# Kernel optimization log

Measured on AMD Instinct MI355X. Metric: run time of the kernel, lower is better.

## Reference

```python
import jax, jax.numpy as jnp
import numpy as np

DT = 1.0            # neuron_config.base_config.dt (ms)
TAU_MEM = 10.0      # membrane time constant (ms)
SURROGATE_BETA = 1.0  # surrogate sigmoid sharpness for spike nonlinearity

B, P = 256, 4096


def setup_inputs() -> dict:
    key = jax.random.key(0)
    k1, k2, k3, k4 = jax.random.split(key, 4)
    return {
        "external_input": jax.random.normal(k1, (B, P), dtype=jnp.float32),
        "lateral_weights": jax.random.normal(k2, (P, P), dtype=jnp.float32) * 0.1,
        "population_activity": jax.random.uniform(k3, (P,), dtype=jnp.float32),
        "v": jax.random.normal(k4, (B, P), dtype=jnp.float32),
        "threshold": jnp.ones((B, P), dtype=jnp.float32),
    }


def reference(external_input, lateral_weights, population_activity, v, threshold):
    P_ = external_input.shape[1]
    # lateral inhibition: zero self-connections (inhibition_mask = eye == 0)
    masked_w = lateral_weights * (1.0 - jnp.eye(P_, dtype=lateral_weights.dtype))
    lateral = population_activity @ masked_w              # [P]
    total_input = external_input - lateral[None, :]        # [B, P]
    # vectorized adaptive-threshold LIF step across the whole population
    decay = jnp.exp(jnp.asarray(-DT / TAU_MEM, dtype=v.dtype))
    v_new = decay * v + total_input                        # [B, P]
    u = (v_new - threshold) / SURROGATE_BETA
    soft = jax.nn.sigmoid(u)
    hard = (v_new > threshold).astype(v.dtype)
    # straight-through spike: hard forward, sigmoid-surrogate gradient
    spikes = jax.lax.stop_gradient(hard - soft) + soft     # [B, P]
    return spikes
```

## Files before the change

kernel.cpp:

```cpp
#include <hip/hip_runtime.h>


#define PP 4096
#define BB 256

using f4 = __attribute__((ext_vector_type(4))) float;

constexpr int ROWS_PER_CHUNK = 16;
constexpr int NCHUNK = PP / ROWS_PER_CHUNK;
constexpr int COLS_PER_TILE = 1024;
constexpr int NTILE = PP / COLS_PER_TILE;

__global__ __launch_bounds__(256)
void lateral_partial(const float* __restrict__ w, const float* __restrict__ pa,
                     double* __restrict__ part) {
    const int tile = blockIdx.x & (NTILE - 1);
    const int rch  = blockIdx.x >> 2;
    const int c    = tile * COLS_PER_TILE + (int)threadIdx.x * 4;
    const int r0   = rch * ROWS_PER_CHUNK;
    double a0 = 0.0, a1 = 0.0, a2 = 0.0, a3 = 0.0;
#pragma unroll
    for (int k = 0; k < ROWS_PER_CHUNK; ++k) {
        const int i = r0 + k;
        const double p = (double)pa[i];
        const f4 wv = __builtin_nontemporal_load(
            reinterpret_cast<const f4*>(w + (size_t)i * PP + c));
        a0 += p * (double)wv.x;
        a1 += p * (double)wv.y;
        a2 += p * (double)wv.z;
        a3 += p * (double)wv.w;
    }
    double* dst = part + (size_t)rch * PP + c;
    *reinterpret_cast<double2*>(dst)     = make_double2(a0, a1);
    *reinterpret_cast<double2*>(dst + 2) = make_double2(a2, a3);
}

__global__ __launch_bounds__(256)
void lateral_reduce(const double* __restrict__ part, const float* __restrict__ w,
                    const float* __restrict__ pa, double* __restrict__ lat) {
    __shared__ double sh[256];
    const int t   = (int)threadIdx.x;
    const int cj  = t & 7;
    const int grp = t >> 3;
    const int col = blockIdx.x * 8 + cj;
    double s = 0.0;
#pragma unroll
    for (int k = 0; k < NCHUNK / 32; ++k)
        s += part[(size_t)(grp * 8 + k) * PP + col];
    sh[t] = s;
    __syncthreads();
#pragma unroll
    for (int off = 128; off >= 8; off >>= 1) {
        if (t < off) sh[t] += sh[t + off];
        __syncthreads();
    }
    if (t < 8) {
        lat[col] = sh[t] - (double)pa[col] * (double)w[(size_t)col * (PP + 1)];
    }
}

__global__ __launch_bounds__(256)
void spike(const float* __restrict__ ext, const float* __restrict__ v,
           const float* __restrict__ thr, const double* __restrict__ lat,
           float* __restrict__ out) {
    const size_t t = ((size_t)blockIdx.x * 256 + threadIdx.x) * 4;
    const int j = (int)(t & (PP - 1));
    const f4 e  = __builtin_nontemporal_load(reinterpret_cast<const f4*>(ext + t));
    const f4 vv = __builtin_nontemporal_load(reinterpret_cast<const f4*>(v + t));
    const f4 th = __builtin_nontemporal_load(reinterpret_cast<const f4*>(thr + t));
    const double l0 = lat[j], l1 = lat[j + 1], l2 = lat[j + 2], l3 = lat[j + 3];
    const double dec = 0.90483741803595952;
    f4 o;
    o.x = (dec * (double)vv.x + (double)e.x - l0 > (double)th.x) ? 1.0f : 0.0f;
    o.y = (dec * (double)vv.y + (double)e.y - l1 > (double)th.y) ? 1.0f : 0.0f;
    o.z = (dec * (double)vv.z + (double)e.z - l2 > (double)th.z) ? 1.0f : 0.0f;
    o.w = (dec * (double)vv.w + (double)e.w - l3 > (double)th.w) ? 1.0f : 0.0f;
    __builtin_nontemporal_store(o, reinterpret_cast<f4*>(out + t));
}

extern "C" void kernel_launch(void* const* d_in, const int* in_sizes, int n_in,
                              void* d_out, int out_size, void* d_ws, size_t ws_size,
                              hipStream_t stream) {
    const float* ext = (const float*)d_in[0];
    const float* w   = (const float*)d_in[1];
    const float* pa  = (const float*)d_in[2];
    const float* v   = (const float*)d_in[3];
    const float* thr = (const float*)d_in[4];
    float* out = (float*)d_out;

    double* part = (double*)d_ws;
    double* lat  = part + (size_t)NCHUNK * PP;

    lateral_partial<<<NTILE * NCHUNK, 256, 0, stream>>>(w, pa, part);
    lateral_reduce<<<PP / 8, 256, 0, stream>>>(part, w, pa, lat);
    spike<<<(BB * PP) / (4 * 256), 256, 0, stream>>>(ext, v, thr, lat, out);
}
```

Before: 120.5 us.

## Fuse lateral reduction into spike kernel and shrink partial-sum buffer

The GEMV partial stage now uses 128-row chunks, with an in-block shared-memory reduction over four 32-row groups, so it writes 32 partial rows instead of 256. The separate reduce and spike kernels are merged: each block reduces partials for 16 columns, subtracts the diagonal term, and applies the spike test over all 256 batch rows for those columns. This removes one launch, the lat round-trip and most of the partial-buffer traffic. In exchange, the spike stage accesses memory in narrow 64-byte column strips per row, which may hurt coalescing, and the nontemporal hints are dropped.

```diff
diff --git a/kernel.cpp b/kernel.cpp
--- a/kernel.cpp
+++ b/kernel.cpp
@@ -6,76 +6,82 @@
 
 using f4 = __attribute__((ext_vector_type(4))) float;
 
-constexpr int ROWS_PER_CHUNK = 16;
-constexpr int NCHUNK = PP / ROWS_PER_CHUNK;
-constexpr int COLS_PER_TILE = 1024;
-constexpr int NTILE = PP / COLS_PER_TILE;
+constexpr int NCHUNK = 32;
+constexpr int NCTILE = 32;
 
 __global__ __launch_bounds__(256)
 void lateral_partial(const float* __restrict__ w, const float* __restrict__ pa,
                      double* __restrict__ part) {
-    const int tile = blockIdx.x & (NTILE - 1);
-    const int rch  = blockIdx.x >> 2;
-    const int c    = tile * COLS_PER_TILE + (int)threadIdx.x * 4;
-    const int r0   = rch * ROWS_PER_CHUNK;
-    double a0 = 0.0, a1 = 0.0, a2 = 0.0, a3 = 0.0;
+    __shared__ double sh[4 * 128];
+    const int tile = blockIdx.x & (NCTILE - 1);
+    const int rch  = blockIdx.x >> 5;
+    const int t    = (int)threadIdx.x;
+    const int cp   = t & 63;
+    const int g    = t >> 6;
+    const int c    = tile * 128 + cp * 2;
+    const int r0   = rch * 128 + g * 32;
+    double a0 = 0.0, a1 = 0.0;
 #pragma unroll
-    for (int k = 0; k < ROWS_PER_CHUNK; ++k) {
+    for (int k = 0; k < 32; ++k) {
         const int i = r0 + k;
         const double p = (double)pa[i];
-        const f4 wv = __builtin_nontemporal_load(
-            reinterpret_cast<const f4*>(w + (size_t)i * PP + c));
+        const float2 wv = *reinterpret_cast<const float2*>(w + (size_t)i * PP + c);
         a0 += p * (double)wv.x;
         a1 += p * (double)wv.y;
-        a2 += p * (double)wv.z;
-        a3 += p * (double)wv.w;
     }
-    double* dst = part + (size_t)rch * PP + c;
-    *reinterpret_cast<double2*>(dst)     = make_double2(a0, a1);
-    *reinterpret_cast<double2*>(dst + 2) = make_double2(a2, a3);
+    sh[g * 128 + cp * 2]     = a0;
+    sh[g * 128 + cp * 2 + 1] = a1;
+    __syncthreads();
+    if (t < 128) {
+        const double s = sh[t] + sh[128 + t] + sh[256 + t] + sh[384 + t];
+        part[(size_t)rch * PP + tile * 128 + t] = s;
+    }
 }
 
-__global__ __launch_bounds__(256)
-void lateral_reduce(const double* __restrict__ part, const float* __restrict__ w,
-                    const float* __restrict__ pa, double* __restrict__ lat) {
-    __shared__ double sh[256];
-    const int t   = (int)threadIdx.x;
-    const int cj  = t & 7;
-    const int grp = t >> 3;
-    const int col = blockIdx.x * 8 + cj;
-    double s = 0.0;
-#pragma unroll
-    for (int k = 0; k < NCHUNK / 32; ++k)
-        s += part[(size_t)(grp * 8 + k) * PP + col];
-    sh[t] = s;
+__global__ __launch_bounds__(512)
+void reduce_spike(const double* __restrict__ part, const float* __restrict__ w,
+                  const float* __restrict__ pa,
+                  const float* __restrict__ ext, const float* __restrict__ v,
+                  const float* __restrict__ thr, float* __restrict__ out) {
+    __shared__ double sh[512];
+    const int t  = (int)threadIdx.x;
+    const int c0 = blockIdx.x * 16;
+
+    {
+        const int cj    = t & 15;
+        const int chunk = t >> 4;
+        sh[t] = part[(size_t)chunk * PP + c0 + cj];
+    }
     __syncthreads();
 #pragma unroll
-    for (int off = 128; off >= 8; off >>= 1) {
+    for (int off = 256; off >= 16; off >>= 1) {
         if (t < off) sh[t] += sh[t + off];
         __syncthreads();
     }
-    if (t < 8) {
-        lat[col] = sh[t] - (double)pa[col] * (double)w[(size_t)col * (PP + 1)];
+    if (t < 16) {
+        const int col = c0 + t;
+        sh[t] -= (double)pa[col] * (double)w[(size_t)col * (PP + 1)];
     }
-}
+    __syncthreads();
 
-__global__ __launch_bounds__(256)
-void spike(const float* __restrict__ ext, const float* __restrict__ v,
-           const float* __restrict__ thr, const double* __restrict__ lat,
-           float* __restrict__ out) {
-    const size_t t = ((size_t)blockIdx.x * 256 + threadIdx.x) * 4;
-    const int j = (int)(t & (PP - 1));
-    const f4 e  = __builtin_nontemporal_load(reinterpret_cast<const f4*>(ext + t));
-    const f4 vv = __builtin_nontemporal_load(reinterpret_cast<const f4*>(v + t));
-    const f4 th = __builtin_nontemporal_load(reinterpret_cast<const f4*>(thr + t));
-    const double l0 = lat[j], l1 = lat[j + 1], l2 = lat[j + 2], l3 = lat[j + 3];
+    const int q  = t & 3;
+    const int r0 = t >> 2;
+    const double l0 = sh[q * 4 + 0], l1 = sh[q * 4 + 1];
+    const double l2 = sh[q * 4 + 2], l3 = sh[q * 4 + 3];
     const double dec = 0.90483741803595952;
-    f4 o;
-    o.x = (dec * (double)vv.x + (double)e.x - l0 > (double)th.x) ? 1.0f : 0.0f;
-    o.y = (dec * (double)vv.y + (double)e.y - l1 > (double)th.y) ? 1.0f : 0.0f;
-    o.z = (dec * (double)vv.z + (double)e.z - l2 > (double)th.z) ? 1.0f : 0.0f;
-    o.w = (dec * (double)vv.w + (double)e.w - l3 > (double)th.w) ? 1.0f : 0.0f;
-    __builtin_nontemporal_store(o, reinterpret_cast<f4*>(out + t));
+#pragma unroll
+    for (int rr = 0; rr < 2; ++rr) {
+        const size_t idx = (size_t)(r0 + rr * 128) * PP + c0 + q * 4;
+        const f4 e  = *reinterpret_cast<const f4*>(ext + idx);
+        const f4 vv = *reinterpret_cast<const f4*>(v + idx);
+        const f4 th = *reinterpret_cast<const f4*>(thr + idx);
+        f4 o;
+        o.x = (dec * (double)vv.x + (double)e.x - l0 > (double)th.x) ? 1.0f : 0.0f;
+        o.y = (dec * (double)vv.y + (double)e.y - l1 > (double)th.y) ? 1.0f : 0.0f;
+        o.z = (dec * (double)vv.z + (double)e.z - l2 > (double)th.z) ? 1.0f : 0.0f;
+        o.w = (dec * (double)vv.w + (double)e.w - l3 > (double)th.w) ? 1.0f : 0.0f;
+        *reinterpret_cast<f4*>(out + idx) = o;
+    }
 }
 
 extern "C" void kernel_launch(void* const* d_in, const int* in_sizes, int n_in,
@@ -89,9 +95,7 @@
     float* out = (float*)d_out;
 
     double* part = (double*)d_ws;
-    double* lat  = part + (size_t)NCHUNK * PP;
 
-    lateral_partial<<<NTILE * NCHUNK, 256, 0, stream>>>(w, pa, part);
-    lateral_reduce<<<PP / 8, 256, 0, stream>>>(part, w, pa, lat);
-    spike<<<(BB * PP) / (4 * 256), 256, 0, stream>>>(ext, v, thr, lat, out);
+    lateral_partial<<<NCTILE * NCHUNK, 256, 0, stream>>>(w, pa, part);
+    reduce_spike<<<PP / 16, 512, 0, stream>>>(part, w, pa, ext, v, thr, out);
 }
```

Result: faster. 113.9 us (-5.5%).
